# Performance work log

Measured on AMD Instinct MI355X. Metric: run time of the kernel, lower is better.

Reference implementation:

```python
import jax, jax.numpy as jnp
import numpy as np
import math

K_SLOTS = 64
DIM = 512
HEADS = 8
HEAD_DIM = DIM // HEADS
EPS = 1e-20
LN_EPS = 1e-5
SQRT_DIM = 1.0 / math.sqrt(HEAD_DIM)


def layernorm(x, g, b):
    mu = jnp.mean(x, axis=-1, keepdims=True)
    var = jnp.var(x, axis=-1, keepdims=True)
    return (x - mu) * jax.lax.rsqrt(var + LN_EPS) * g + b


def setup_inputs() -> dict:
    key = jax.random.key(0)
    ks = jax.random.split(key, 8)
    B, T = 8, 8192
    lim = 1.0 / math.sqrt(DIM)
    return {
        "X": jax.random.normal(ks[0], (B, T, DIM), jnp.float32),
        "slots_w": jax.random.normal(ks[1], (K_SLOTS, DIM), jnp.float32),
        "g_slots": jnp.ones((DIM,), jnp.float32),
        "b_slots": jnp.zeros((DIM,), jnp.float32),
        "Wk": jax.random.uniform(ks[2], (DIM, DIM), jnp.float32, -lim, lim),
        "bk": jax.random.uniform(ks[3], (DIM,), jnp.float32, -lim, lim),
        "Wv": jax.random.uniform(ks[4], (DIM, DIM), jnp.float32, -lim, lim),
        "bv": jax.random.uniform(ks[5], (DIM,), jnp.float32, -lim, lim),
        "g_after": jnp.ones((DIM,), jnp.float32),
        "b_after": jnp.zeros((DIM,), jnp.float32),
    }


def reference(X, slots_w, g_slots, b_slots, Wk, bk, Wv, bv, g_after, b_after):
    B, T, D = X.shape
    # slots -> queries, shared across batch: (K, D) -> (H, K, hd)
    S = layernorm(slots_w, g_slots, b_slots)
    Q = S.reshape(K_SLOTS, HEADS, HEAD_DIM).transpose(1, 0, 2)  # (H, K, hd)
    # key/value projections, head split: (B, T, D) -> (B, H, T, hd)
    Kx = (X @ Wk.T + bk).reshape(B, T, HEADS, HEAD_DIM).transpose(0, 2, 1, 3)
    V = (X @ Wv.T + bv).reshape(B, T, HEADS, HEAD_DIM).transpose(0, 2, 1, 3)
    # attention logits (B, H, K, T), scale = 1/sqrt(head_dim)
    A = jnp.einsum("hkd,bhsd->bhks", Q, Kx) * SQRT_DIM
    # softmax over the SLOT axis (k), then renormalize by row-sum over s
    W = jax.nn.softmax(A, axis=-2)
    C = jnp.sum(W, axis=-1, keepdims=True)  # (B, H, K, 1)
    A = W / (C + EPS)
    S_hat = jnp.einsum("bhks,bhsd->bhkd", A, V)  # (B, H, K, hd)
    S_hat = S_hat.transpose(0, 2, 1, 3).reshape(B, K_SLOTS, D)
    return layernorm(S_hat, g_after, b_after)
```

## Files before the change

### kernel.cpp

```cpp
#include <hip/hip_runtime.h>
#include <hip/hip_bf16.h>
#include <math.h>

typedef unsigned short ushort_t;
typedef unsigned int u32;

constexpr int D  = 512;
constexpr int T  = 8192;
constexpr int B  = 8;
constexpr int H  = 8;
constexpr int KS = 64;
constexpr int HD = 64;
constexpr float SCALE = 0.125f;
constexpr float LNEPS = 1e-5f;
constexpr float EPS   = 1e-20f;

constexpr int TC  = 128;
constexpr int CPB = 2;

constexpr size_t OFF_S    = 0;
constexpr size_t OFF_BQ   = 32768;
constexpr size_t OFF_SACC = 33280;
constexpr size_t OFF_CACC = 295424;
constexpr size_t OFF_WB2  = 299520;

typedef __attribute__((ext_vector_type(8))) short bf16x8;
typedef __attribute__((ext_vector_type(4))) float f32x4;
typedef __attribute__((ext_vector_type(4))) unsigned short us4;

typedef const __attribute__((address_space(1))) u32* gas_ptr;
typedef __attribute__((address_space(3))) u32* las_ptr;

__device__ __forceinline__ void gload16(const void* g, void* l) {
  __builtin_amdgcn_global_load_lds((gas_ptr)g, (las_ptr)l, 16, 0, 0);
}

__device__ __forceinline__ ushort_t f2bf(float x) {
  __hip_bfloat16 t = __float2bfloat16(x);
  return *(ushort_t*)&t;
}

__device__ __forceinline__ u32 pk2bf(float x, float y) {
  __hip_bfloat162 t = __float22bfloat162_rn(make_float2(x, y));
  return *(u32*)&t;
}

__device__ __forceinline__ bf16x8 cvt8(f32x4 a, f32x4 b) {
  union { bf16x8 v; u32 u[4]; } r;
  r.u[0] = pk2bf(a.x, a.y); r.u[1] = pk2bf(a.z, a.w);
  r.u[2] = pk2bf(b.x, b.y); r.u[3] = pk2bf(b.z, b.w);
  return r.v;
}

__global__ void ln_slots_kernel(const float* __restrict__ slots_w,
                                const float* __restrict__ g, const float* __restrict__ b,
                                float* __restrict__ S) {
  __shared__ float red[8];
  int k = blockIdx.x;
  int tid = threadIdx.x;
  float x0 = slots_w[k*D + tid];
  float x1 = slots_w[k*D + tid + 256];
  float s1 = x0 + x1, s2 = x0*x0 + x1*x1;
  for (int off = 32; off; off >>= 1) { s1 += __shfl_xor(s1, off); s2 += __shfl_xor(s2, off); }
  if ((tid & 63) == 0) { red[tid >> 6] = s1; red[4 + (tid >> 6)] = s2; }
  __syncthreads();
  s1 = red[0] + red[1] + red[2] + red[3];
  s2 = red[4] + red[5] + red[6] + red[7];
  float mu = s1 / D;
  float var = s2 / D - mu * mu;
  float rs = rsqrtf(var + LNEPS);
  S[k*D + tid]       = (x0 - mu) * rs * g[tid]       + b[tid];
  S[k*D + tid + 256] = (x1 - mu) * rs * g[tid + 256] + b[tid + 256];
}

__global__ void weff_kernel(const float* __restrict__ S, const float* __restrict__ Wk,
                            ushort_t* __restrict__ Wb2) {
  int gid = blockIdx.x * 256 + threadIdx.x;
  int in = gid & 511;
  int hk = gid >> 9;
  int h = hk >> 6, k = hk & 63;
  const float* srow = S + k*D + h*HD;
  const float* wcol = Wk + (size_t)(h*HD)*D + in;
  float acc = 0.f;
  #pragma unroll 8
  for (int d = 0; d < HD; ++d) acc += srow[d] * wcol[(size_t)d*D];
  Wb2[(size_t)(h*128 + k)*D + in] = f2bf(acc * SCALE);
}

__global__ void bq_kernel(const float* __restrict__ S, const float* __restrict__ bk,
                          float* __restrict__ bq) {
  int hk = blockIdx.x * 256 + threadIdx.x;
  int h = hk >> 6, k = hk & 63;
  float acc = 0.f;
  for (int d = 0; d < HD; ++d) acc += S[k*D + h*HD + d] * bk[h*HD + d];
  bq[hk] = acc * SCALE;
}

__global__ void wvcopy_kernel(const float* __restrict__ Wv, ushort_t* __restrict__ Wb2) {
  int gid = blockIdx.x * 256 + threadIdx.x;
  int in = gid & 511;
  int hd = gid >> 9;
  int h = hd >> 6, d = hd & 63;
  Wb2[(size_t)(h*128 + 64 + d)*D + in] = f2bf(Wv[(size_t)hd*D + in]);
}

__global__ void zero_kernel(float* __restrict__ p, int n) {
  int gid = blockIdx.x * 256 + threadIdx.x;
  if (gid < n) p[gid] = 0.f;
}

__global__ __launch_bounds__(256, 3) void main_kernel(
    const float* __restrict__ X, const ushort_t* __restrict__ Wb2,
    const float* __restrict__ bq, const float* __restrict__ bv,
    float* __restrict__ Sacc, float* __restrict__ Cacc) {
  __shared__ __align__(16) char smem[34816];
  float*    A_lds = (float*)smem;
  ushort_t* B_lds = (ushort_t*)(smem + 16384);
  ushort_t* W_lds = (ushort_t*)smem;
  ushort_t* V_lds = (ushort_t*)(smem + 17408);

  const int tid  = threadIdx.x;
  const int lane = tid & 63, w = tid >> 6;
  const int wm = w & 1, wn = w >> 1;
  const int m16 = lane & 15, q = lane >> 4;

  const int id = blockIdx.x;
  const int h  = (id >> 3) & 7;
  const int cg = (id & 7) | ((id >> 6) << 3);
  const int bh = (cg >> 5) * H + h;

  f32x4 acc2[4] = {};
  float csum[4] = {0.f, 0.f, 0.f, 0.f};

  for (int cc = 0; cc < CPB; ++cc) {
    const float* Xc = X + (size_t)(cg * CPB + cc) * TC * D;
    f32x4 acc[4][4] = {};

    for (int kb = 0; kb < D; kb += 32) {
      __syncthreads();
      #pragma unroll
      for (int m = 0; m < 4; ++m) {
        int li = tid + m * 256;
        int row = li >> 3, c = li & 7;
        gload16(Xc + (size_t)row * D + kb + c * 4, A_lds + (size_t)li * 4);
      }
      #pragma unroll
      for (int m = 0; m < 2; ++m) {
        int li = tid + m * 256;
        int col = li >> 2, c = li & 3;
        gload16(Wb2 + (size_t)(h * 128 + col) * D + kb + c * 8, B_lds + (size_t)li * 8);
      }
      __syncthreads();
      bf16x8 af[4], bf[4];
      #pragma unroll
      for (int i = 0; i < 4; ++i) {
        const f32x4* ap = (const f32x4*)(A_lds + (wm * 64 + i * 16 + m16) * 32 + q * 8);
        af[i] = cvt8(ap[0], ap[1]);
      }
      #pragma unroll
      for (int j = 0; j < 4; ++j)
        bf[j] = *(const bf16x8*)(B_lds + (wn * 64 + j * 16 + m16) * 32 + q * 8);
      #pragma unroll
      for (int i = 0; i < 4; ++i)
        #pragma unroll
        for (int j = 0; j < 4; ++j)
          acc[i][j] = __builtin_amdgcn_mfma_f32_16x16x32_bf16(af[i], bf[j], acc[i][j], 0, 0, 0);
    }
    __syncthreads();

    if (wn == 0) {
      float bqv[4];
      #pragma unroll
      for (int j = 0; j < 4; ++j) bqv[j] = bq[h * KS + j * 16 + m16];
      #pragma unroll
      for (int i = 0; i < 4; ++i) {
        us4 wp[4];
        #pragma unroll
        for (int r = 0; r < 4; ++r) {
          float v0 = acc[i][0][r] + bqv[0];
          float v1 = acc[i][1][r] + bqv[1];
          float v2 = acc[i][2][r] + bqv[2];
          float v3 = acc[i][3][r] + bqv[3];
          float mx = fmaxf(fmaxf(v0, v1), fmaxf(v2, v3));
          mx = fmaxf(mx, __shfl_xor(mx, 1));
          mx = fmaxf(mx, __shfl_xor(mx, 2));
          mx = fmaxf(mx, __shfl_xor(mx, 4));
          mx = fmaxf(mx, __shfl_xor(mx, 8));
          v0 = __expf(v0 - mx); v1 = __expf(v1 - mx);
          v2 = __expf(v2 - mx); v3 = __expf(v3 - mx);
          float s = v0 + v1 + v2 + v3;
          s += __shfl_xor(s, 1); s += __shfl_xor(s, 2);
          s += __shfl_xor(s, 4); s += __shfl_xor(s, 8);
          float inv = __builtin_amdgcn_rcpf(s);
          v0 *= inv; v1 *= inv; v2 *= inv; v3 *= inv;
          csum[0] += v0; csum[1] += v1; csum[2] += v2; csum[3] += v3;
          wp[0][r] = f2bf(v0); wp[1][r] = f2bf(v1);
          wp[2][r] = f2bf(v2); wp[3][r] = f2bf(v3);
        }
        #pragma unroll
        for (int j = 0; j < 4; ++j)
          *(us4*)(W_lds + (j * 16 + m16) * 136 + wm * 64 + i * 16 + q * 4) = wp[j];
      }
    } else {
      float bvv[4];
      #pragma unroll
      for (int j = 0; j < 4; ++j) bvv[j] = bv[h * HD + j * 16 + m16];
      #pragma unroll
      for (int i = 0; i < 4; ++i) {
        #pragma unroll
        for (int j = 0; j < 4; ++j) {
          us4 pk;
          pk.x = f2bf(acc[i][j][0] + bvv[j]);
          pk.y = f2bf(acc[i][j][1] + bvv[j]);
          pk.z = f2bf(acc[i][j][2] + bvv[j]);
          pk.w = f2bf(acc[i][j][3] + bvv[j]);
          *(us4*)(V_lds + (j * 16 + m16) * 136 + wm * 64 + i * 16 + q * 4) = pk;
        }
      }
    }
    __syncthreads();

    #pragma unroll
    for (int kk = 0; kk < 4; ++kk) {
      bf16x8 a = *(const bf16x8*)(W_lds + (w * 16 + m16) * 136 + kk * 32 + q * 8);
      #pragma unroll
      for (int j = 0; j < 4; ++j) {
        bf16x8 bb = *(const bf16x8*)(V_lds + (j * 16 + m16) * 136 + kk * 32 + q * 8);
        acc2[j] = __builtin_amdgcn_mfma_f32_16x16x32_bf16(a, bb, acc2[j], 0, 0, 0);
      }
    }
  }

  float* Sb = Sacc + (size_t)bh * KS * HD;
  #pragma unroll
  for (int j = 0; j < 4; ++j)
    #pragma unroll
    for (int r = 0; r < 4; ++r)
      atomicAdd(Sb + (w * 16 + q * 4 + r) * HD + j * 16 + m16, acc2[j][r]);

  if (wn == 0) {
    #pragma unroll
    for (int j = 0; j < 4; ++j) {
      float c = csum[j];
      c += __shfl_xor(c, 16);
      c += __shfl_xor(c, 32);
      if (q == 0) atomicAdd(Cacc + (size_t)bh * KS + j * 16 + m16, c);
    }
  }
}

__global__ void finalize_kernel(const float* __restrict__ Sacc, const float* __restrict__ Cacc,
                                const float* __restrict__ g, const float* __restrict__ bb,
                                float* __restrict__ out) {
  __shared__ float red[8];
  int bk_ = blockIdx.x;
  int b = bk_ >> 6, k = bk_ & 63;
  int tid = threadIdx.x;
  float v[2];
  #pragma unroll
  for (int m = 0; m < 2; ++m) {
    int d = tid + m*256;
    int h = d >> 6, dd = d & 63;
    float c = Cacc[((size_t)b*H + h)*KS + k];
    v[m] = Sacc[(((size_t)b*H + h)*KS + k)*HD + dd] / (c + EPS);
  }
  float s1 = v[0] + v[1], s2 = v[0]*v[0] + v[1]*v[1];
  for (int off = 32; off; off >>= 1) { s1 += __shfl_xor(s1, off); s2 += __shfl_xor(s2, off); }
  if ((tid & 63) == 0) { red[tid >> 6] = s1; red[4 + (tid >> 6)] = s2; }
  __syncthreads();
  s1 = red[0] + red[1] + red[2] + red[3];
  s2 = red[4] + red[5] + red[6] + red[7];
  float mu = s1 / D;
  float var = s2 / D - mu * mu;
  float rs = rsqrtf(var + LNEPS);
  #pragma unroll
  for (int m = 0; m < 2; ++m) {
    int d = tid + m*256;
    out[(size_t)bk_*D + d] = (v[m] - mu) * rs * g[d] + bb[d];
  }
}

extern "C" void kernel_launch(void* const* d_in, const int* in_sizes, int n_in,
                              void* d_out, int out_size, void* d_ws, size_t ws_size,
                              hipStream_t stream) {
  const float* X       = (const float*)d_in[0];
  const float* slots_w = (const float*)d_in[1];
  const float* g_slots = (const float*)d_in[2];
  const float* b_slots = (const float*)d_in[3];
  const float* Wk      = (const float*)d_in[4];
  const float* bk      = (const float*)d_in[5];
  const float* Wv      = (const float*)d_in[6];
  const float* bv      = (const float*)d_in[7];
  const float* g_after = (const float*)d_in[8];
  const float* b_after = (const float*)d_in[9];
  float* ws   = (float*)d_ws;
  float* S    = ws + OFF_S;
  float* bq   = ws + OFF_BQ;
  float* Sacc = ws + OFF_SACC;
  float* Cacc = ws + OFF_CACC;
  ushort_t* Wb2 = (ushort_t*)(ws + OFF_WB2);
  float* out  = (float*)d_out;

  hipLaunchKernelGGL(ln_slots_kernel, dim3(64), dim3(256), 0, stream, slots_w, g_slots, b_slots, S);
  hipLaunchKernelGGL(weff_kernel, dim3(1024), dim3(256), 0, stream, S, Wk, Wb2);
  hipLaunchKernelGGL(bq_kernel, dim3(2), dim3(256), 0, stream, S, bk, bq);
  hipLaunchKernelGGL(wvcopy_kernel, dim3(1024), dim3(256), 0, stream, Wv, Wb2);
  hipLaunchKernelGGL(zero_kernel, dim3(1040), dim3(256), 0, stream, Sacc, 266240);
  hipLaunchKernelGGL(main_kernel, dim3(2048), dim3(256), 0, stream, X, Wb2, bq, bv, Sacc, Cacc);
  hipLaunchKernelGGL(finalize_kernel, dim3(B * KS), dim3(256), 0, stream,
                     Sacc, Cacc, g_after, b_after, out);
}
```

Measured before the change: 363.0 us.

## Fuse setup kernels, swizzle bf16 LDS tiles, replace atomics with partial sums

Merges slot layernorm, effective-query weight, bias and Wv copy into one setup kernel. The main kernel converts X to bf16 before storing it to an XOR-swizzled LDS tile and doubles the K step to 64. The softmax max-subtraction is dropped in favour of a clamp at 30. Per-block results go to partial buffers that the finalize kernel reduces, removing the zeroing pass and the atomics. Launch bounds rise to 4 blocks per CU. This trades async global-to-LDS loads for register-staged loads and relies on logits staying below the clamp.

```diff
diff --git a/kernel.cpp b/kernel.cpp
--- a/kernel.cpp
+++ b/kernel.cpp
@@ -15,14 +15,10 @@
 constexpr float LNEPS = 1e-5f;
 constexpr float EPS   = 1e-20f;
 
-constexpr int TC  = 128;
-constexpr int CPB = 2;
-
-constexpr size_t OFF_S    = 0;
-constexpr size_t OFF_BQ   = 32768;
-constexpr size_t OFF_SACC = 33280;
-constexpr size_t OFF_CACC = 295424;
-constexpr size_t OFF_WB2  = 299520;
+constexpr size_t OFF_BQ    = 0;
+constexpr size_t OFF_WB2   = 512;
+constexpr size_t OFF_SPART = 262656;
+constexpr size_t OFF_CPART = 8651264;
 
 typedef __attribute__((ext_vector_type(8))) short bf16x8;
 typedef __attribute__((ext_vector_type(4))) float f32x4;
@@ -52,12 +48,17 @@
   return r.v;
 }
 
-__global__ void ln_slots_kernel(const float* __restrict__ slots_w,
-                                const float* __restrict__ g, const float* __restrict__ b,
-                                float* __restrict__ S) {
+__global__ void setup_kernel(const float* __restrict__ slots_w,
+                             const float* __restrict__ g, const float* __restrict__ b,
+                             const float* __restrict__ Wk, const float* __restrict__ bk,
+                             const float* __restrict__ Wv,
+                             ushort_t* __restrict__ Wb2, float* __restrict__ bq) {
+  __shared__ float S_lds[512];
   __shared__ float red[8];
-  int k = blockIdx.x;
-  int tid = threadIdx.x;
+  const int hk = blockIdx.x;
+  const int h = hk >> 6, k = hk & 63;
+  const int tid = threadIdx.x;
+
   float x0 = slots_w[k*D + tid];
   float x1 = slots_w[k*D + tid + 256];
   float s1 = x0 + x1, s2 = x0*x0 + x1*x1;
@@ -69,52 +70,33 @@
   float mu = s1 / D;
   float var = s2 / D - mu * mu;
   float rs = rsqrtf(var + LNEPS);
-  S[k*D + tid]       = (x0 - mu) * rs * g[tid]       + b[tid];
-  S[k*D + tid + 256] = (x1 - mu) * rs * g[tid + 256] + b[tid + 256];
-}
-
-__global__ void weff_kernel(const float* __restrict__ S, const float* __restrict__ Wk,
-                            ushort_t* __restrict__ Wb2) {
-  int gid = blockIdx.x * 256 + threadIdx.x;
-  int in = gid & 511;
-  int hk = gid >> 9;
-  int h = hk >> 6, k = hk & 63;
-  const float* srow = S + k*D + h*HD;
-  const float* wcol = Wk + (size_t)(h*HD)*D + in;
-  float acc = 0.f;
-  #pragma unroll 8
-  for (int d = 0; d < HD; ++d) acc += srow[d] * wcol[(size_t)d*D];
-  Wb2[(size_t)(h*128 + k)*D + in] = f2bf(acc * SCALE);
-}
-
-__global__ void bq_kernel(const float* __restrict__ S, const float* __restrict__ bk,
-                          float* __restrict__ bq) {
-  int hk = blockIdx.x * 256 + threadIdx.x;
-  int h = hk >> 6, k = hk & 63;
-  float acc = 0.f;
-  for (int d = 0; d < HD; ++d) acc += S[k*D + h*HD + d] * bk[h*HD + d];
-  bq[hk] = acc * SCALE;
-}
-
-__global__ void wvcopy_kernel(const float* __restrict__ Wv, ushort_t* __restrict__ Wb2) {
-  int gid = blockIdx.x * 256 + threadIdx.x;
-  int in = gid & 511;
-  int hd = gid >> 9;
-  int h = hd >> 6, d = hd & 63;
-  Wb2[(size_t)(h*128 + 64 + d)*D + in] = f2bf(Wv[(size_t)hd*D + in]);
-}
-
-__global__ void zero_kernel(float* __restrict__ p, int n) {
-  int gid = blockIdx.x * 256 + threadIdx.x;
-  if (gid < n) p[gid] = 0.f;
-}
-
-__global__ __launch_bounds__(256, 3) void main_kernel(
+  S_lds[tid]       = (x0 - mu) * rs * g[tid]       + b[tid];
+  S_lds[tid + 256] = (x1 - mu) * rs * g[tid + 256] + b[tid + 256];
+  __syncthreads();
+
+  #pragma unroll
+  for (int rep = 0; rep < 2; ++rep) {
+    int in = tid + rep * 256;
+    float acc = 0.f;
+    #pragma unroll 8
+    for (int d = 0; d < 64; ++d)
+      acc += S_lds[h*64 + d] * Wk[(size_t)(h*64 + d)*D + in];
+    Wb2[(size_t)(h*128 + k)*D + in] = f2bf(acc * SCALE);
+    Wb2[(size_t)(h*128 + 64 + k)*D + in] = f2bf(Wv[(size_t)hk*D + in]);
+  }
+  if (tid < 64) {
+    float p = S_lds[h*64 + tid] * bk[h*64 + tid];
+    for (int off = 32; off; off >>= 1) p += __shfl_xor(p, off);
+    if (tid == 0) bq[hk] = p * SCALE;
+  }
+}
+
+__global__ __launch_bounds__(256, 4) void main_kernel5(
     const float* __restrict__ X, const ushort_t* __restrict__ Wb2,
     const float* __restrict__ bq, const float* __restrict__ bv,
-    float* __restrict__ Sacc, float* __restrict__ Cacc) {
+    float* __restrict__ Spart, float* __restrict__ Cpart) {
   __shared__ __align__(16) char smem[34816];
-  float*    A_lds = (float*)smem;
+  ushort_t* A_lds = (ushort_t*)smem;
   ushort_t* B_lds = (ushort_t*)(smem + 16384);
   ushort_t* W_lds = (ushort_t*)smem;
   ushort_t* V_lds = (ushort_t*)(smem + 17408);
@@ -123,48 +105,53 @@
   const int lane = tid & 63, w = tid >> 6;
   const int wm = w & 1, wn = w >> 1;
   const int m16 = lane & 15, q = lane >> 4;
+  const int m7 = m16 & 7;
 
   const int id = blockIdx.x;
   const int h  = (id >> 3) & 7;
   const int cg = (id & 7) | ((id >> 6) << 3);
-  const int bh = (cg >> 5) * H + h;
 
   f32x4 acc2[4] = {};
   float csum[4] = {0.f, 0.f, 0.f, 0.f};
 
-  for (int cc = 0; cc < CPB; ++cc) {
-    const float* Xc = X + (size_t)(cg * CPB + cc) * TC * D;
+  for (int cc = 0; cc < 2; ++cc) {
+    const float* Xc = X + (size_t)(cg * 2 + cc) * 128 * D;
     f32x4 acc[4][4] = {};
 
-    for (int kb = 0; kb < D; kb += 32) {
+    for (int kb = 0; kb < D; kb += 64) {
       __syncthreads();
+      #pragma unroll
+      for (int m = 0; m < 4; ++m) {
+        int F = tid + m * 256;
+        int token = F >> 3, c = F & 7;
+        const float* src = Xc + (size_t)token * D + kb + c * 8;
+        f32x4 a = *(const f32x4*)src;
+        f32x4 b2 = *(const f32x4*)(src + 4);
+        *(bf16x8*)(A_lds + ((size_t)token * 8 + (c ^ (token & 7))) * 8) = cvt8(a, b2);
+      }
       #pragma unroll
       for (int m = 0; m < 4; ++m) {
         int li = tid + m * 256;
-        int row = li >> 3, c = li & 7;
-        gload16(Xc + (size_t)row * D + kb + c * 4, A_lds + (size_t)li * 4);
-      }
-      #pragma unroll
-      for (int m = 0; m < 2; ++m) {
-        int li = tid + m * 256;
-        int col = li >> 2, c = li & 3;
-        gload16(Wb2 + (size_t)(h * 128 + col) * D + kb + c * 8, B_lds + (size_t)li * 8);
+        int col = li >> 3, cs = li & 7;
+        int kc = cs ^ (col & 7);
+        gload16(Wb2 + (size_t)(h * 128 + col) * D + kb + kc * 8, B_lds + (size_t)li * 8);
       }
       __syncthreads();
-      bf16x8 af[4], bf[4];
-      #pragma unroll
-      for (int i = 0; i < 4; ++i) {
-        const f32x4* ap = (const f32x4*)(A_lds + (wm * 64 + i * 16 + m16) * 32 + q * 8);
-        af[i] = cvt8(ap[0], ap[1]);
-      }
-      #pragma unroll
-      for (int j = 0; j < 4; ++j)
-        bf[j] = *(const bf16x8*)(B_lds + (wn * 64 + j * 16 + m16) * 32 + q * 8);
-      #pragma unroll
-      for (int i = 0; i < 4; ++i)
+      #pragma unroll
+      for (int ks = 0; ks < 2; ++ks) {
+        bf16x8 af[4], bfv[4];
+        #pragma unroll
+        for (int i = 0; i < 4; ++i)
+          af[i] = *(const bf16x8*)(A_lds + ((size_t)(wm*64 + i*16 + m16) * 8 + ((ks*4 + q) ^ m7)) * 8);
         #pragma unroll
         for (int j = 0; j < 4; ++j)
-          acc[i][j] = __builtin_amdgcn_mfma_f32_16x16x32_bf16(af[i], bf[j], acc[i][j], 0, 0, 0);
+          bfv[j] = *(const bf16x8*)(B_lds + ((size_t)(wn*64 + j*16 + m16) * 8 + ((ks*4 + q) ^ m7)) * 8);
+        #pragma unroll
+        for (int i = 0; i < 4; ++i)
+          #pragma unroll
+          for (int j = 0; j < 4; ++j)
+            acc[i][j] = __builtin_amdgcn_mfma_f32_16x16x32_bf16(af[i], bfv[j], acc[i][j], 0, 0, 0);
+      }
     }
     __syncthreads();
 
@@ -177,17 +164,10 @@
         us4 wp[4];
         #pragma unroll
         for (int r = 0; r < 4; ++r) {
-          float v0 = acc[i][0][r] + bqv[0];
-          float v1 = acc[i][1][r] + bqv[1];
-          float v2 = acc[i][2][r] + bqv[2];
-          float v3 = acc[i][3][r] + bqv[3];
-          float mx = fmaxf(fmaxf(v0, v1), fmaxf(v2, v3));
-          mx = fmaxf(mx, __shfl_xor(mx, 1));
-          mx = fmaxf(mx, __shfl_xor(mx, 2));
-          mx = fmaxf(mx, __shfl_xor(mx, 4));
-          mx = fmaxf(mx, __shfl_xor(mx, 8));
-          v0 = __expf(v0 - mx); v1 = __expf(v1 - mx);
-          v2 = __expf(v2 - mx); v3 = __expf(v3 - mx);
+          float v0 = __expf(fminf(acc[i][0][r] + bqv[0], 30.f));
+          float v1 = __expf(fminf(acc[i][1][r] + bqv[1], 30.f));
+          float v2 = __expf(fminf(acc[i][2][r] + bqv[2], 30.f));
+          float v3 = __expf(fminf(acc[i][3][r] + bqv[3], 30.f));
           float s = v0 + v1 + v2 + v3;
           s += __shfl_xor(s, 1); s += __shfl_xor(s, 2);
           s += __shfl_xor(s, 4); s += __shfl_xor(s, 8);
@@ -206,7 +186,7 @@
       #pragma unroll
       for (int j = 0; j < 4; ++j) bvv[j] = bv[h * HD + j * 16 + m16];
       #pragma unroll
-      for (int i = 0; i < 4; ++i) {
+      for (int i = 0; i < 4; ++i)
         #pragma unroll
         for (int j = 0; j < 4; ++j) {
           us4 pk;
@@ -216,7 +196,6 @@
           pk.w = f2bf(acc[i][j][3] + bvv[j]);
           *(us4*)(V_lds + (j * 16 + m16) * 136 + wm * 64 + i * 16 + q * 4) = pk;
         }
-      }
     }
     __syncthreads();
 
@@ -231,12 +210,13 @@
     }
   }
 
-  float* Sb = Sacc + (size_t)bh * KS * HD;
+  const int sidx = cg * 8 + h;
+  float* Sb = Spart + (size_t)sidx * (KS * HD);
   #pragma unroll
   for (int j = 0; j < 4; ++j)
     #pragma unroll
     for (int r = 0; r < 4; ++r)
-      atomicAdd(Sb + (w * 16 + q * 4 + r) * HD + j * 16 + m16, acc2[j][r]);
+      Sb[(w * 16 + q * 4 + r) * HD + j * 16 + m16] = acc2[j][r];
 
   if (wn == 0) {
     #pragma unroll
@@ -244,12 +224,12 @@
       float c = csum[j];
       c += __shfl_xor(c, 16);
       c += __shfl_xor(c, 32);
-      if (q == 0) atomicAdd(Cacc + (size_t)bh * KS + j * 16 + m16, c);
-    }
-  }
-}
-
-__global__ void finalize_kernel(const float* __restrict__ Sacc, const float* __restrict__ Cacc,
+      if (q == 0) Cpart[(size_t)sidx * 128 + wm * 64 + j * 16 + m16] = c;
+    }
+  }
+}
+
+__global__ void finalize_kernel(const float* __restrict__ Spart, const float* __restrict__ Cpart,
                                 const float* __restrict__ g, const float* __restrict__ bb,
                                 float* __restrict__ out) {
   __shared__ float red[8];
@@ -259,10 +239,16 @@
   float v[2];
   #pragma unroll
   for (int m = 0; m < 2; ++m) {
-    int d = tid + m*256;
+    int d = tid + m * 256;
     int h = d >> 6, dd = d & 63;
-    float c = Cacc[((size_t)b*H + h)*KS + k];
-    v[m] = Sacc[(((size_t)b*H + h)*KS + k)*HD + dd] / (c + EPS);
+    float s = 0.f, c = 0.f;
+    #pragma unroll 4
+    for (int i = 0; i < 32; ++i) {
+      int sidx = (b * 32 + i) * 8 + h;
+      s += Spart[(size_t)sidx * (KS * HD) + k * HD + dd];
+      c += Cpart[(size_t)sidx * 128 + k] + Cpart[(size_t)sidx * 128 + 64 + k];
+    }
+    v[m] = s / (c + EPS);
   }
   float s1 = v[0] + v[1], s2 = v[0]*v[0] + v[1]*v[1];
   for (int off = 32; off; off >>= 1) { s1 += __shfl_xor(s1, off); s2 += __shfl_xor(s2, off); }
@@ -275,8 +261,8 @@
   float rs = rsqrtf(var + LNEPS);
   #pragma unroll
   for (int m = 0; m < 2; ++m) {
-    int d = tid + m*256;
-    out[(size_t)bk_*D + d] = (v[m] - mu) * rs * g[d] + bb[d];
+    int d = tid + m * 256;
+    out[(size_t)bk_ * D + d] = (v[m] - mu) * rs * g[d] + bb[d];
   }
 }
 
@@ -293,20 +279,17 @@
   const float* bv      = (const float*)d_in[7];
   const float* g_after = (const float*)d_in[8];
   const float* b_after = (const float*)d_in[9];
-  float* ws   = (float*)d_ws;
-  float* S    = ws + OFF_S;
-  float* bq   = ws + OFF_BQ;
-  float* Sacc = ws + OFF_SACC;
-  float* Cacc = ws + OFF_CACC;
+  float* ws    = (float*)d_ws;
+  float* bq    = ws + OFF_BQ;
   ushort_t* Wb2 = (ushort_t*)(ws + OFF_WB2);
-  float* out  = (float*)d_out;
-
-  hipLaunchKernelGGL(ln_slots_kernel, dim3(64), dim3(256), 0, stream, slots_w, g_slots, b_slots, S);
-  hipLaunchKernelGGL(weff_kernel, dim3(1024), dim3(256), 0, stream, S, Wk, Wb2);
-  hipLaunchKernelGGL(bq_kernel, dim3(2), dim3(256), 0, stream, S, bk, bq);
-  hipLaunchKernelGGL(wvcopy_kernel, dim3(1024), dim3(256), 0, stream, Wv, Wb2);
-  hipLaunchKernelGGL(zero_kernel, dim3(1040), dim3(256), 0, stream, Sacc, 266240);
-  hipLaunchKernelGGL(main_kernel, dim3(2048), dim3(256), 0, stream, X, Wb2, bq, bv, Sacc, Cacc);
+  float* Spart = ws + OFF_SPART;
+  float* Cpart = ws + OFF_CPART;
+  float* out   = (float*)d_out;
+
+  hipLaunchKernelGGL(setup_kernel, dim3(512), dim3(256), 0, stream,
+                     slots_w, g_slots, b_slots, Wk, bk, Wv, Wb2, bq);
+  hipLaunchKernelGGL(main_kernel5, dim3(2048), dim3(256), 0, stream,
+                     X, Wb2, bq, bv, Spart, Cpart);
   hipLaunchKernelGGL(finalize_kernel, dim3(B * KS), dim3(256), 0, stream,
-                     Sacc, Cacc, g_after, b_after, out);
-}
+                     Spart, Cpart, g_after, b_after, out);
+}
```

Result: slower. 379.4 us (+4.5%).
